# Kernel optimization log

Hardware: AMD Instinct MI355X
Metric: run time of the kernel (lower is better)

The kernel has to match this reference:

```python
import jax, jax.numpy as jnp
import numpy as np

NEG_INF = -2.0**32 + 1.0  # matches torch paddings value


def prelu(x, a):
    return jnp.where(x >= 0, x, a * x)


def setup_inputs() -> dict:
    key = jax.random.key(0)
    ks = jax.random.split(key, 12)
    B, L, D, A = 2048, 200, 128, 64
    return {
        "query": jax.random.normal(ks[0], (B, D), jnp.float32),
        "keys": jax.random.normal(ks[1], (B, L, D), jnp.float32),
        "keys_length": jax.random.randint(ks[2], (B,), 0, L, jnp.int64 if jax.config.jax_enable_x64 else jnp.int32),
        "W1": jax.random.normal(ks[3], (4 * D, A), jnp.float32) * (1.0 / np.sqrt(4 * D)),
        "b1": jax.random.normal(ks[4], (A,), jnp.float32) * 0.01,
        "a1": jnp.full((1,), 0.25, jnp.float32),  # PReLU default init
        "W2": jax.random.normal(ks[5], (A, A), jnp.float32) * (1.0 / np.sqrt(A)),
        "b2": jax.random.normal(ks[6], (A,), jnp.float32) * 0.01,
        "a2": jnp.full((1,), 0.25, jnp.float32),
        "W3": jax.random.normal(ks[7], (A, 1), jnp.float32) * (1.0 / np.sqrt(A)),
        "b3": jax.random.normal(ks[8], (1,), jnp.float32) * 0.01,
    }


def reference(query, keys, keys_length, W1, b1, a1, W2, b2, a2, W3, b3):
    B, L, D = keys.shape
    q = jnp.broadcast_to(query[:, None, :], (B, L, D))
    # concat features: [q, k, q-k, q*k] -> (B, L, 4D)
    q_k = jnp.concatenate([q, keys, q - keys, q * keys], axis=-1)
    h = prelu(jnp.einsum("blf,fa->bla", q_k, W1) + b1, a1)
    h = prelu(jnp.einsum("bla,ac->blc", h, W2) + b2, a2)
    scores = (jnp.einsum("bla,ao->blo", h, W3) + b3)[..., 0]  # (B, L)
    mask = jnp.arange(L)[None, :] < keys_length[:, None]
    scores = jnp.where(mask, scores, NEG_INF)
    att = jax.nn.softmax(scores, axis=1)
    out = jnp.einsum("bl,bld->bd", att, keys)  # bmm(att[:,None,:], keys)
    return out, att
```

## Files before the change

### kernel.cpp

```cpp
#include <hip/hip_runtime.h>
#include <math.h>

typedef __attribute__((ext_vector_type(8))) _Float16 half8;
typedef __attribute__((ext_vector_type(4))) float float4_t;

#define NB 2048
#define LL 200
#define DD 128
#define AA 64
#define NEG_INF_F -4294967295.0f

#define WQ_STRIDE 136

#define WS_WBC_H  0
#define WS_W1D_H  8704
#define WS_W2T_H  17408
#define WS_QA_OFF 43008

__global__ __launch_bounds__(256)
void din_prep(const float* __restrict__ query,
              const float* __restrict__ W1,
              const float* __restrict__ b1,
              const float* __restrict__ W2,
              _Float16* __restrict__ ws16,
              float* __restrict__ qa)
{
    const int tid = threadIdx.x;
    const int blk = blockIdx.x;

    if (blk < 128) {
        __shared__ float sW1s[DD * AA];
        __shared__ float sq[16 * DD];
        const int b0 = blk * 16;
        for (int i = tid; i < DD * AA; i += 256)
            sW1s[i] = W1[i] + W1[2 * DD * AA + i];
        for (int i = tid; i < 16 * DD; i += 256)
            sq[i] = query[(size_t)b0 * DD + i];
        __syncthreads();
        const int lane = tid & 63, bb = tid >> 6;
        for (int g = 0; g < 4; ++g) {
            const int bi = bb * 4 + g;
            float acc = b1[lane];
            #pragma unroll 8
            for (int d = 0; d < DD; ++d)
                acc += sq[bi * DD + d] * sW1s[d * AA + lane];
            qa[(size_t)(b0 + bi) * AA + lane] = acc;
        }
    } else if (blk == 128) {
        for (int i = tid; i < 64 * 17; i += 256) {
            const int a = i / 17, c = i - a * 17;
            half8 hb, hd;
            if (c == 16) {
                #pragma unroll
                for (int j = 0; j < 8; ++j) { hb[j] = (_Float16)0.f; hd[j] = (_Float16)0.f; }
            } else {
                const int d0 = c * 8;
                #pragma unroll
                for (int j = 0; j < 8; ++j) {
                    const int d = d0 + j;
                    hb[j] = (_Float16)(W1[(DD + d) * AA + a] - W1[(2 * DD + d) * AA + a]);
                    hd[j] = (_Float16)(W1[(3 * DD + d) * AA + a]);
                }
            }
            *(half8*)&ws16[WS_WBC_H + a * WQ_STRIDE + c * 8] = hb;
            *(half8*)&ws16[WS_W1D_H + a * WQ_STRIDE + c * 8] = hd;
        }
    } else {
        _Float16* w2t = ws16 + WS_W2T_H;
        const int c = tid >> 2, j0 = (tid & 3) * 16;
        for (int ch = 0; ch < 2; ++ch) {
            half8 v;
            #pragma unroll
            for (int j = 0; j < 8; ++j)
                v[j] = (_Float16)W2[(j0 + ch * 8 + j) * AA + c];
            *(half8*)&w2t[c * AA + j0 + ch * 8] = v;
        }
    }
}

__global__ __launch_bounds__(256, 3)
void din_main(const float* __restrict__ keys,
              const int*   __restrict__ keys_length,
              const float* __restrict__ a1p,
              const float* __restrict__ b2,
              const float* __restrict__ a2p,
              const float* __restrict__ W3,
              const _Float16* __restrict__ ws16,
              const float* __restrict__ qa,
              const float* __restrict__ query,
              float* __restrict__ out,
              float* __restrict__ att)
{
    __shared__ __align__(16) _Float16 sWq[AA * WQ_STRIDE];
    __shared__ __align__(16) _Float16 sTile[4 * 16 * DD];
    __shared__ __align__(16) _Float16 sH1[4 * 16 * 72];
    __shared__ float sQ[136];
    __shared__ float sS[224];
    __shared__ float sML[16];
    __shared__ float sRed[16];

    const int tid  = threadIdx.x;
    const int lane = tid & 63, wv = tid >> 6;
    const int col  = lane & 15, quad = lane >> 4;
    const int b    = blockIdx.x;
    const int len  = keys_length[b];
    const float pa1 = a1p[0], pa2 = a2p[0];

    if (tid < 136) sQ[tid] = (tid < 128) ? query[(size_t)b * DD + tid] : 0.f;
    for (int i = tid; i < 224; i += 256) sS[i] = NEG_INF_F;
    __syncthreads();

    for (int ci = tid; ci < 64 * 17; ci += 256) {
        const int c = ci % 17;
        const int d0 = c * 8;
        const half8 hb = *(const half8*)&ws16[WS_WBC_H + ci * 8];
        const half8 hd = *(const half8*)&ws16[WS_W1D_H + ci * 8];
        half8 r;
        #pragma unroll
        for (int j = 0; j < 8; ++j)
            r[j] = (_Float16)((float)hb[j] + sQ[d0 + j] * (float)hd[j]);
        *(half8*)&sWq[ci * 8] = r;
    }
    __syncthreads();

    const _Float16* w2t = ws16 + WS_W2T_H;
    half8 w2f[2][4];
    #pragma unroll
    for (int ks = 0; ks < 2; ++ks)
        #pragma unroll
        for (int n = 0; n < 4; ++n)
            w2f[ks][n] = *(const half8*)&w2t[(n * 16 + col) * AA + ks * 32 + quad * 8];
    float qareg[4], b2reg[4], w3reg[4];
    #pragma unroll
    for (int n = 0; n < 4; ++n) {
        qareg[n] = qa[(size_t)b * AA + n * 16 + col];
        b2reg[n] = b2[n * 16 + col];
        w3reg[n] = W3[n * 16 + col];
    }

    const int ntiles = (len + 15) >> 4;
    _Float16* const myTile = &sTile[wv * 16 * DD];
    _Float16* const myH    = &sH1[wv * 16 * 72];

    float m_run = -INFINITY;
    float O[8];
    #pragma unroll
    for (int j = 0; j < 8; ++j) O[j] = 0.f;

    for (int t = wv; t < ntiles; t += 4) {
        const int l0 = t * 16;

        #pragma unroll
        for (int it = 0; it < 4; ++it) {
            const int i = lane + 64 * it;
            const int row = i >> 4, c8 = i & 15;
            const int l = l0 + row;
            const int lr = (l < LL) ? l : (LL - 1);
            const float* kp = keys + ((size_t)b * LL + lr) * DD + c8 * 8;
            const float4 v0 = *(const float4*)kp;
            const float4 v1 = *(const float4*)(kp + 4);
            half8 h;
            h[0] = (_Float16)v0.x; h[1] = (_Float16)v0.y; h[2] = (_Float16)v0.z; h[3] = (_Float16)v0.w;
            h[4] = (_Float16)v1.x; h[5] = (_Float16)v1.y; h[6] = (_Float16)v1.z; h[7] = (_Float16)v1.w;
            *(half8*)&myTile[row * DD + ((c8 ^ (row & 7)) << 3)] = h;
        }

        float4_t C[4] = {{0,0,0,0},{0,0,0,0},{0,0,0,0},{0,0,0,0}};
        #pragma unroll
        for (int ks = 0; ks < 4; ++ks) {
            const half8 af = *(const half8*)&myTile[col * DD + (((ks * 4 + quad) ^ (col & 7)) << 3)];
            const int ko = ks * 32 + quad * 8;
            #pragma unroll
            for (int n = 0; n < 4; ++n) {
                const half8 bf = *(const half8*)&sWq[(n * 16 + col) * WQ_STRIDE + ko];
                C[n] = __builtin_amdgcn_mfma_f32_16x16x32_f16(af, bf, C[n], 0, 0, 0);
            }
        }
        #pragma unroll
        for (int n = 0; n < 4; ++n)
            #pragma unroll
            for (int r = 0; r < 4; ++r) {
                float v = C[n][r] + qareg[n];
                v = v >= 0.f ? v : pa1 * v;
                myH[(quad * 4 + r) * 72 + n * 16 + col] = (_Float16)v;
            }
        float4_t D[4] = {{0,0,0,0},{0,0,0,0},{0,0,0,0},{0,0,0,0}};
        #pragma unroll
        for (int ks = 0; ks < 2; ++ks) {
            const half8 af = *(const half8*)&myH[col * 72 + ks * 32 + quad * 8];
            #pragma unroll
            for (int n = 0; n < 4; ++n)
                D[n] = __builtin_amdgcn_mfma_f32_16x16x32_f16(af, w2f[ks][n], D[n], 0, 0, 0);
        }
        float pr[4] = {0.f, 0.f, 0.f, 0.f};
        #pragma unroll
        for (int n = 0; n < 4; ++n)
            #pragma unroll
            for (int r = 0; r < 4; ++r) {
                float v = D[n][r] + b2reg[n];
                v = v >= 0.f ? v : pa2 * v;
                pr[r] += v * w3reg[n];
            }
        float sv[4];
        #pragma unroll
        for (int r = 0; r < 4; ++r) {
            float pv = pr[r];
            pv += __shfl_xor(pv, 1);
            pv += __shfl_xor(pv, 2);
            pv += __shfl_xor(pv, 4);
            pv += __shfl_xor(pv, 8);
            const int l = l0 + quad * 4 + r;
            const bool valid = (l < len);
            sv[r] = valid ? pv : -INFINITY;
            if (col == 0 && valid) sS[l] = pv;
        }
        const float tmax = fmaxf(fmaxf(sv[0], sv[1]), fmaxf(sv[2], sv[3]));
        const float newm = fmaxf(m_run, tmax);
        if (newm != -INFINITY) {
            const float alpha = expf(m_run - newm);
            #pragma unroll
            for (int j = 0; j < 8; ++j) O[j] *= alpha;
            #pragma unroll
            for (int r = 0; r < 4; ++r) {
                const float e = (sv[r] == -INFINITY) ? 0.f : expf(sv[r] - newm);
                const int rr = quad * 4 + r;
                const half8 kv = *(const half8*)&myTile[rr * DD + ((col ^ (rr & 7)) << 3)];
                #pragma unroll
                for (int j = 0; j < 8; ++j) O[j] += e * (float)kv[j];
            }
            m_run = newm;
        }
    }

    float* const myO = (float*)myH;
    #pragma unroll
    for (int j = 0; j < 8; ++j) myO[quad * 128 + col * 8 + j] = O[j];
    if (col == 0) sML[wv * 4 + quad] = m_run;
    __syncthreads();

    float m = (tid < LL) ? sS[tid] : -INFINITY;
    #pragma unroll
    for (int o = 1; o < 64; o <<= 1) m = fmaxf(m, __shfl_xor(m, o));
    if (lane == 0) sRed[wv] = m;
    __syncthreads();
    const float M = fmaxf(fmaxf(sRed[0], sRed[1]), fmaxf(sRed[2], sRed[3]));
    float e = (tid < LL) ? expf(sS[tid] - M) : 0.f;
    float s = e;
    #pragma unroll
    for (int o = 1; o < 64; o <<= 1) s += __shfl_xor(s, o);
    if (lane == 0) sRed[8 + wv] = s;
    __syncthreads();
    const float S = sRed[8] + sRed[9] + sRed[10] + sRed[11];
    const float inv = 1.f / S;
    if (tid < LL) att[(size_t)b * LL + tid] = e * inv;

    if (tid < 16) sML[tid] = expf(sML[tid] - M);
    __syncthreads();

    if (len > 0) {
        if (tid < DD) {
            const float* fO = (const float*)sH1;
            float r = 0.f;
            #pragma unroll
            for (int w = 0; w < 4; ++w)
                #pragma unroll
                for (int q = 0; q < 4; ++q)
                    r += sML[w * 4 + q] * fO[w * 576 + q * 128 + tid];
            out[(size_t)b * DD + tid] = r * inv;
        }
    } else {
        const int d = tid & 127, ph = tid >> 7;
        float acc = 0.f;
        for (int l = ph; l < LL; l += 2)
            acc += keys[((size_t)b * LL + l) * DD + d];
        float* const sc = (float*)sTile;
        sc[tid] = acc;
        __syncthreads();
        if (tid < DD)
            out[(size_t)b * DD + tid] = (sc[tid] + sc[tid + 128]) * (1.f / 200.f);
    }
}

extern "C" void kernel_launch(void* const* d_in, const int* in_sizes, int n_in,
                              void* d_out, int out_size, void* d_ws, size_t ws_size,
                              hipStream_t stream) {
    (void)in_sizes; (void)n_in; (void)ws_size; (void)out_size;
    const float* query = (const float*)d_in[0];
    const float* keys  = (const float*)d_in[1];
    const int*   klen  = (const int*)d_in[2];
    const float* W1    = (const float*)d_in[3];
    const float* b1    = (const float*)d_in[4];
    const float* a1    = (const float*)d_in[5];
    const float* W2    = (const float*)d_in[6];
    const float* b2    = (const float*)d_in[7];
    const float* a2    = (const float*)d_in[8];
    const float* W3    = (const float*)d_in[9];

    _Float16* ws16 = (_Float16*)d_ws;
    float*    qawk = (float*)((char*)d_ws + WS_QA_OFF);

    float* out = (float*)d_out;
    float* att = out + (size_t)NB * DD;

    hipLaunchKernelGGL(din_prep, dim3(130), dim3(256), 0, stream,
                       query, W1, b1, W2, ws16, qawk);
    hipLaunchKernelGGL(din_main, dim3(NB), dim3(256), 0, stream,
                       keys, klen, a1, b2, a2, W3, ws16, qawk, query, out, att);
}
```

Before: 361.5 us.

## Double-buffer 64-row key chunks with register prefetch across the block

The main kernel now stages keys in 64-row chunks shared by all four waves. A double-buffered LDS layout holds the chunks, and the next chunk is prefetched into registers while MFMA work runs on the current one. The first chunk load is issued before the Wq setup, so it overlaps global latency with that setup. This adds a block-wide barrier per chunk, roughly doubles key LDS use, and lowers the launch-bounds occupancy hint from 3 to 2. The prep kernel is also split into 512 smaller blocks for more parallelism.

After: 337.6 us. 1.07x faster.

```diff
diff --git a/kernel.cpp b/kernel.cpp
--- a/kernel.cpp
+++ b/kernel.cpp
@@ -28,25 +28,22 @@
     const int tid = threadIdx.x;
     const int blk = blockIdx.x;
 
-    if (blk < 128) {
+    if (blk < 512) {
         __shared__ float sW1s[DD * AA];
-        __shared__ float sq[16 * DD];
-        const int b0 = blk * 16;
+        __shared__ float sq[4 * DD];
+        const int b0 = blk * 4;
         for (int i = tid; i < DD * AA; i += 256)
             sW1s[i] = W1[i] + W1[2 * DD * AA + i];
-        for (int i = tid; i < 16 * DD; i += 256)
+        for (int i = tid; i < 4 * DD; i += 256)
             sq[i] = query[(size_t)b0 * DD + i];
         __syncthreads();
-        const int lane = tid & 63, bb = tid >> 6;
-        for (int g = 0; g < 4; ++g) {
-            const int bi = bb * 4 + g;
-            float acc = b1[lane];
-            #pragma unroll 8
-            for (int d = 0; d < DD; ++d)
-                acc += sq[bi * DD + d] * sW1s[d * AA + lane];
-            qa[(size_t)(b0 + bi) * AA + lane] = acc;
-        }
-    } else if (blk == 128) {
+        const int lane = tid & 63, bi = tid >> 6;
+        float acc = b1[lane];
+        #pragma unroll 8
+        for (int d = 0; d < DD; ++d)
+            acc += sq[bi * DD + d] * sW1s[d * AA + lane];
+        qa[(size_t)(b0 + bi) * AA + lane] = acc;
+    } else if (blk == 512) {
         for (int i = tid; i < 64 * 17; i += 256) {
             const int a = i / 17, c = i - a * 17;
             half8 hb, hd;
@@ -78,7 +75,7 @@
     }
 }
 
-__global__ __launch_bounds__(256, 3)
+__global__ __launch_bounds__(256, 2)
 void din_main(const float* __restrict__ keys,
               const int*   __restrict__ keys_length,
               const float* __restrict__ a1p,
@@ -91,8 +88,8 @@
               float* __restrict__ out,
               float* __restrict__ att)
 {
+    __shared__ __align__(16) _Float16 sKb[2][64 * DD];
     __shared__ __align__(16) _Float16 sWq[AA * WQ_STRIDE];
-    __shared__ __align__(16) _Float16 sTile[4 * 16 * DD];
     __shared__ __align__(16) _Float16 sH1[4 * 16 * 72];
     __shared__ float sQ[136];
     __shared__ float sS[224];
@@ -105,7 +102,20 @@
     const int b    = blockIdx.x;
     const int len  = keys_length[b];
     const float pa1 = a1p[0], pa2 = a2p[0];
-
+    const int nch = (len + 63) >> 6;
+
+    float4 pfa[4], pfb[4];
+    if (nch > 0) {
+        #pragma unroll
+        for (int it = 0; it < 4; ++it) {
+            const int i = tid + it * 256;
+            int rg = i >> 4;
+            rg = (rg < len) ? rg : (len - 1);
+            const float* kp = keys + ((size_t)b * LL + rg) * DD + (i & 15) * 8;
+            pfa[it] = *(const float4*)kp;
+            pfb[it] = *(const float4*)(kp + 4);
+        }
+    }
     if (tid < 136) sQ[tid] = (tid < 128) ? query[(size_t)b * DD + tid] : 0.f;
     for (int i = tid; i < 224; i += 256) sS[i] = NEG_INF_F;
     __syncthreads();
@@ -121,8 +131,19 @@
             r[j] = (_Float16)((float)hb[j] + sQ[d0 + j] * (float)hd[j]);
         *(half8*)&sWq[ci * 8] = r;
     }
-    __syncthreads();
-
+    if (nch > 0) {
+        #pragma unroll
+        for (int it = 0; it < 4; ++it) {
+            const int i = tid + it * 256;
+            const int row = i >> 4, c8 = i & 15;
+            half8 h;
+            h[0] = (_Float16)pfa[it].x; h[1] = (_Float16)pfa[it].y;
+            h[2] = (_Float16)pfa[it].z; h[3] = (_Float16)pfa[it].w;
+            h[4] = (_Float16)pfb[it].x; h[5] = (_Float16)pfb[it].y;
+            h[6] = (_Float16)pfb[it].z; h[7] = (_Float16)pfb[it].w;
+            *(half8*)&sKb[0][row * DD + ((c8 ^ (row & 7)) << 3)] = h;
+        }
+    }
     const _Float16* w2t = ws16 + WS_W2T_H;
     half8 w2f[2][4];
     #pragma unroll
@@ -137,99 +158,112 @@
         b2reg[n] = b2[n * 16 + col];
         w3reg[n] = W3[n * 16 + col];
     }
-
-    const int ntiles = (len + 15) >> 4;
-    _Float16* const myTile = &sTile[wv * 16 * DD];
-    _Float16* const myH    = &sH1[wv * 16 * 72];
+    __syncthreads();
 
     float m_run = -INFINITY;
     float O[8];
     #pragma unroll
     for (int j = 0; j < 8; ++j) O[j] = 0.f;
-
-    for (int t = wv; t < ntiles; t += 4) {
-        const int l0 = t * 16;
-
-        #pragma unroll
-        for (int it = 0; it < 4; ++it) {
-            const int i = lane + 64 * it;
-            const int row = i >> 4, c8 = i & 15;
-            const int l = l0 + row;
-            const int lr = (l < LL) ? l : (LL - 1);
-            const float* kp = keys + ((size_t)b * LL + lr) * DD + c8 * 8;
-            const float4 v0 = *(const float4*)kp;
-            const float4 v1 = *(const float4*)(kp + 4);
-            half8 h;
-            h[0] = (_Float16)v0.x; h[1] = (_Float16)v0.y; h[2] = (_Float16)v0.z; h[3] = (_Float16)v0.w;
-            h[4] = (_Float16)v1.x; h[5] = (_Float16)v1.y; h[6] = (_Float16)v1.z; h[7] = (_Float16)v1.w;
-            *(half8*)&myTile[row * DD + ((c8 ^ (row & 7)) << 3)] = h;
-        }
-
-        float4_t C[4] = {{0,0,0,0},{0,0,0,0},{0,0,0,0},{0,0,0,0}};
-        #pragma unroll
-        for (int ks = 0; ks < 4; ++ks) {
-            const half8 af = *(const half8*)&myTile[col * DD + (((ks * 4 + quad) ^ (col & 7)) << 3)];
-            const int ko = ks * 32 + quad * 8;
-            #pragma unroll
-            for (int n = 0; n < 4; ++n) {
-                const half8 bf = *(const half8*)&sWq[(n * 16 + col) * WQ_STRIDE + ko];
-                C[n] = __builtin_amdgcn_mfma_f32_16x16x32_f16(af, bf, C[n], 0, 0, 0);
-            }
-        }
-        #pragma unroll
-        for (int n = 0; n < 4; ++n)
+    _Float16* const myH = &sH1[wv * 16 * 72];
+
+    for (int c = 0; c < nch; ++c) {
+        const bool more = (c + 1 < nch);
+        if (more) {
+            #pragma unroll
+            for (int it = 0; it < 4; ++it) {
+                const int i = tid + it * 256;
+                int rg = (c + 1) * 64 + (i >> 4);
+                rg = (rg < len) ? rg : (len - 1);
+                const float* kp = keys + ((size_t)b * LL + rg) * DD + (i & 15) * 8;
+                pfa[it] = *(const float4*)kp;
+                pfb[it] = *(const float4*)(kp + 4);
+            }
+        }
+        const _Float16* const buf = sKb[c & 1];
+        const int l0 = c * 64 + wv * 16;
+        if (l0 < len) {
+            const int lrow = wv * 16 + col;
+
+            float4_t C[4] = {{0,0,0,0},{0,0,0,0},{0,0,0,0},{0,0,0,0}};
+            #pragma unroll
+            for (int ks = 0; ks < 4; ++ks) {
+                const half8 af = *(const half8*)&buf[lrow * DD + (((ks * 4 + quad) ^ (col & 7)) << 3)];
+                const int ko = ks * 32 + quad * 8;
+                #pragma unroll
+                for (int n = 0; n < 4; ++n) {
+                    const half8 bf = *(const half8*)&sWq[(n * 16 + col) * WQ_STRIDE + ko];
+                    C[n] = __builtin_amdgcn_mfma_f32_16x16x32_f16(af, bf, C[n], 0, 0, 0);
+                }
+            }
+            #pragma unroll
+            for (int n = 0; n < 4; ++n)
+                #pragma unroll
+                for (int r = 0; r < 4; ++r) {
+                    float v = C[n][r] + qareg[n];
+                    v = v >= 0.f ? v : pa1 * v;
+                    myH[(quad * 4 + r) * 72 + n * 16 + col] = (_Float16)v;
+                }
+            float4_t D[4] = {{0,0,0,0},{0,0,0,0},{0,0,0,0},{0,0,0,0}};
+            #pragma unroll
+            for (int ks = 0; ks < 2; ++ks) {
+                const half8 af = *(const half8*)&myH[col * 72 + ks * 32 + quad * 8];
+                #pragma unroll
+                for (int n = 0; n < 4; ++n)
+                    D[n] = __builtin_amdgcn_mfma_f32_16x16x32_f16(af, w2f[ks][n], D[n], 0, 0, 0);
+            }
+            float pr[4] = {0.f, 0.f, 0.f, 0.f};
+            #pragma unroll
+            for (int n = 0; n < 4; ++n)
+                #pragma unroll
+                for (int r = 0; r < 4; ++r) {
+                    float v = D[n][r] + b2reg[n];
+                    v = v >= 0.f ? v : pa2 * v;
+                    pr[r] += v * w3reg[n];
+                }
+            float sv[4];
             #pragma unroll
             for (int r = 0; r < 4; ++r) {
-                float v = C[n][r] + qareg[n];
-                v = v >= 0.f ? v : pa1 * v;
-                myH[(quad * 4 + r) * 72 + n * 16 + col] = (_Float16)v;
-            }
-        float4_t D[4] = {{0,0,0,0},{0,0,0,0},{0,0,0,0},{0,0,0,0}};
-        #pragma unroll
-        for (int ks = 0; ks < 2; ++ks) {
-            const half8 af = *(const half8*)&myH[col * 72 + ks * 32 + quad * 8];
-            #pragma unroll
-            for (int n = 0; n < 4; ++n)
-                D[n] = __builtin_amdgcn_mfma_f32_16x16x32_f16(af, w2f[ks][n], D[n], 0, 0, 0);
-        }
-        float pr[4] = {0.f, 0.f, 0.f, 0.f};
-        #pragma unroll
-        for (int n = 0; n < 4; ++n)
-            #pragma unroll
-            for (int r = 0; r < 4; ++r) {
-                float v = D[n][r] + b2reg[n];
-                v = v >= 0.f ? v : pa2 * v;
-                pr[r] += v * w3reg[n];
-            }
-        float sv[4];
-        #pragma unroll
-        for (int r = 0; r < 4; ++r) {
-            float pv = pr[r];
-            pv += __shfl_xor(pv, 1);
-            pv += __shfl_xor(pv, 2);
-            pv += __shfl_xor(pv, 4);
-            pv += __shfl_xor(pv, 8);
-            const int l = l0 + quad * 4 + r;
-            const bool valid = (l < len);
-            sv[r] = valid ? pv : -INFINITY;
-            if (col == 0 && valid) sS[l] = pv;
-        }
-        const float tmax = fmaxf(fmaxf(sv[0], sv[1]), fmaxf(sv[2], sv[3]));
-        const float newm = fmaxf(m_run, tmax);
-        if (newm != -INFINITY) {
-            const float alpha = expf(m_run - newm);
-            #pragma unroll
-            for (int j = 0; j < 8; ++j) O[j] *= alpha;
-            #pragma unroll
-            for (int r = 0; r < 4; ++r) {
-                const float e = (sv[r] == -INFINITY) ? 0.f : expf(sv[r] - newm);
-                const int rr = quad * 4 + r;
-                const half8 kv = *(const half8*)&myTile[rr * DD + ((col ^ (rr & 7)) << 3)];
-                #pragma unroll
-                for (int j = 0; j < 8; ++j) O[j] += e * (float)kv[j];
-            }
-            m_run = newm;
-        }
+                float pv = pr[r];
+                pv += __shfl_xor(pv, 1);
+                pv += __shfl_xor(pv, 2);
+                pv += __shfl_xor(pv, 4);
+                pv += __shfl_xor(pv, 8);
+                const int l = l0 + quad * 4 + r;
+                const bool valid = (l < len);
+                sv[r] = valid ? pv : -INFINITY;
+                if (col == 0 && valid) sS[l] = pv;
+            }
+            const float tmax = fmaxf(fmaxf(sv[0], sv[1]), fmaxf(sv[2], sv[3]));
+            const float newm = fmaxf(m_run, tmax);
+            if (newm != -INFINITY) {
+                const float alpha = expf(m_run - newm);
+                #pragma unroll
+                for (int j = 0; j < 8; ++j) O[j] *= alpha;
+                #pragma unroll
+                for (int r = 0; r < 4; ++r) {
+                    const float e = (sv[r] == -INFINITY) ? 0.f : expf(sv[r] - newm);
+                    const int rr = wv * 16 + quad * 4 + r;
+                    const half8 kv = *(const half8*)&buf[rr * DD + ((col ^ (rr & 7)) << 3)];
+                    #pragma unroll
+                    for (int j = 0; j < 8; ++j) O[j] += e * (float)kv[j];
+                }
+                m_run = newm;
+            }
+        }
+        if (more) {
+            #pragma unroll
+            for (int it = 0; it < 4; ++it) {
+                const int i = tid + it * 256;
+                const int row = i >> 4, c8 = i & 15;
+                half8 h;
+                h[0] = (_Float16)pfa[it].x; h[1] = (_Float16)pfa[it].y;
+                h[2] = (_Float16)pfa[it].z; h[3] = (_Float16)pfa[it].w;
+                h[4] = (_Float16)pfb[it].x; h[5] = (_Float16)pfb[it].y;
+                h[6] = (_Float16)pfb[it].z; h[7] = (_Float16)pfb[it].w;
+                *(half8*)&sKb[(c + 1) & 1][row * DD + ((c8 ^ (row & 7)) << 3)] = h;
+            }
+        }
+        __syncthreads();
     }
 
     float* const myO = (float*)myH;
@@ -273,7 +307,7 @@
         float acc = 0.f;
         for (int l = ph; l < LL; l += 2)
             acc += keys[((size_t)b * LL + l) * DD + d];
-        float* const sc = (float*)sTile;
+        float* const sc = (float*)sKb[0];
         sc[tid] = acc;
         __syncthreads();
         if (tid < DD)
@@ -302,7 +336,7 @@
     float* out = (float*)d_out;
     float* att = out + (size_t)NB * DD;
 
-    hipLaunchKernelGGL(din_prep, dim3(130), dim3(256), 0, stream,
+    hipLaunchKernelGGL(din_prep, dim3(514), dim3(256), 0, stream,
                        query, W1, b1, W2, ws16, qawk);
     hipLaunchKernelGGL(din_main, dim3(NB), dim3(256), 0, stream,
                        keys, klen, a1, b2, a2, W3, ws16, qawk, query, out, att);
```
